# Optimization experiments

Hardware: AMD Instinct MI355X
Metric: run time of the kernel (lower is better)

Reference implementation:

```python
import jax, jax.numpy as jnp
import numpy as np

F_OUT = 256      # out_channels
NH = 8           # num_heads
DH = F_OUT // NH # head dim = 32
KH = KW = 8      # kernel (window) size == stride == q_stride
KK = KH * KW     # 64 keys per window


def setup_inputs() -> dict:
    key = jax.random.key(0)
    k1, k2, k3 = jax.random.split(key, 3)
    x = jax.random.normal(k1, (8, 256, 128, 128), jnp.float32)
    # 1x1 conv weight for qkv projection, xavier-ish scale
    proj_w = jax.random.normal(k2, (3 * F_OUT, 256), jnp.float32) * (1.0 / np.sqrt(256.0))
    proj_b = jnp.zeros((3 * F_OUT,), jnp.float32)
    # learned position features (module inits to zeros; use small random for a nontrivial test)
    pos_feats = jax.random.normal(k3, (F_OUT, KK), jnp.float32) * 0.02
    return {"x": x, "proj_w": proj_w, "proj_b": proj_b, "pos_feats": pos_feats}


def reference(x, proj_w, proj_b, pos_feats):
    B, C, H, W = x.shape
    f = F_OUT
    # 1x1 conv == channel GEMM: [B,3f,H,W]
    qkv = jnp.einsum('bchw,oc->bohw', x, proj_w) + proj_b[None, :, None, None]
    scale = float(f // NH) ** (-0.25)
    # query: slice every q_stride-th position -> [B,f,Hq,Wq]
    q = qkv[:, :f, ::KH, ::KW]
    kv = qkv[:, f:3 * f]                       # [B,2f,H,W]
    Hq, Wq = H // KH, W // KW
    # non-overlapping window unfold (stride==kernel, padding=0, dilation=1)
    # -> [B,Hq,Wq,2f,KK], matching torch as_strided(...).reshape(..., -1)
    kv = kv.reshape(B, 2 * f, Hq, KH, Wq, KW)
    kv = kv.transpose(0, 2, 4, 1, 3, 5).reshape(B, Hq, Wq, 2 * f, KK)
    # keys: pos_feats + scale*key, then split heads -> [B,Hq,Wq,NH,DH,KK]
    key_m = (pos_feats + scale * kv[..., :f, :]).reshape(B, Hq, Wq, NH, DH, KK)
    val_m = kv[..., f:2 * f, :].reshape(B, Hq, Wq, NH, DH, KK)
    # queries: scale, channels-last, split heads -> [B,Hq,Wq,NH,DH]
    q_m = (scale * q).transpose(0, 2, 3, 1).reshape(B, Hq, Wq, NH, DH)
    logits = jnp.einsum('bhwnd,bhwndk->bhwnk', q_m, key_m)   # [B,Hq,Wq,NH,KK]
    attn = jax.nn.softmax(logits, axis=-1)
    out = jnp.einsum('bhwnk,bhwndk->bhwnd', attn, val_m)     # [B,Hq,Wq,NH,DH]
    return out.reshape(B, Hq, Wq, f).transpose(0, 3, 1, 2)   # [B,f,Hq,Wq]
```

## Files before the change

kernel.cpp:

```cpp
#include <hip/hip_runtime.h>
#include <hip/hip_bf16.h>
#include <cstdint>
#include <cstddef>

#define SCALE 0.42044820762685725f

typedef __attribute__((ext_vector_type(8))) short short8;
typedef __attribute__((ext_vector_type(4))) short short4v;
typedef __attribute__((ext_vector_type(4))) float f32x4;

__device__ __forceinline__ unsigned int pk2bf(float lo, float hi) {
    __hip_bfloat162 h = __float22bfloat162_rn(float2{lo, hi});
    unsigned int u;
    __builtin_memcpy(&u, &h, sizeof(u));
    return u;
}
__device__ __forceinline__ unsigned short f2bf(float f) {
    unsigned int u = __builtin_bit_cast(unsigned int, f);
    u = (u + 0x7fffu + ((u >> 16) & 1u)) >> 16;
    return (unsigned short)u;
}
__device__ __forceinline__ float bf2f(unsigned short h) {
    unsigned int u = ((unsigned int)h) << 16;
    return __builtin_bit_cast(float, u);
}


__global__ __launch_bounds__(256) void prepack_w(const float* __restrict__ w,
                                                 const float* __restrict__ pos,
                                                 unsigned short* __restrict__ wp,
                                                 unsigned short* __restrict__ pT,
                                                 float* __restrict__ wqT) {
    int gid = blockIdx.x * 256 + threadIdx.x;
    if (gid < 24576) {
        int lane = gid & 63;
        int ks   = (gid >> 6) & 7;
        int mtg  = gid >> 9;
        int row  = (mtg < 32 ? 256 + mtg * 16 : (mtg - 32) * 16) + (lane & 15);
        int k0   = ks * 32 + (lane >> 4) * 8;
        const float* src = w + row * 256 + k0;
        short8 v;
#pragma unroll
        for (int j = 0; j < 8; ++j) v[j] = (short)f2bf(src[j]);
        *reinterpret_cast<short8*>(wp + (size_t)gid * 8) = v;
    } else if (gid < 40960) {
        int u = gid - 24576;
        pT[u] = f2bf(pos[(u & 255) * 64 + (u >> 8)]);
    } else {
        int u = gid - 40960;
        wqT[u] = w[(u & 255) * 256 + (u >> 8)];
    }
}

__global__ __launch_bounds__(256) void q_kernel(const float* __restrict__ x,
                                                const float* __restrict__ wqT,
                                                const float* __restrict__ proj_b,
                                                float* __restrict__ q_all) {
    __shared__ float s_x0[16][256];
    const int t = threadIdx.x;
    const int tile0 = blockIdx.x * 16;
    const int b = tile0 >> 8, hq = (tile0 >> 4) & 15;
    {
        const float* src = x + (size_t)b * 4194304 + (size_t)t * 16384 + hq * 1024;
#pragma unroll
        for (int j = 0; j < 16; ++j) s_x0[j][t] = src[j * 8];
    }
    __syncthreads();
    float acc[16];
#pragma unroll
    for (int j = 0; j < 16; ++j) acc[j] = 0.f;
#pragma unroll 4
    for (int c = 0; c < 256; ++c) {
        float wv = wqT[c * 256 + t];
#pragma unroll
        for (int j = 0; j < 16; ++j) acc[j] = fmaf(wv, s_x0[j][c], acc[j]);
    }
    float bq = proj_b[t];
#pragma unroll
    for (int j = 0; j < 16; ++j)
        q_all[(size_t)(tile0 + j) * 256 + t] = SCALE * (acc[j] + bq);
}

template <bool PRE>
__global__ __launch_bounds__(512, 2) void attn_fused(
        const float* __restrict__ x, const float* __restrict__ proj_w,
        const float* __restrict__ proj_b, const float* __restrict__ pos,
        const unsigned short* __restrict__ wpack, const unsigned short* __restrict__ posT,
        const float* __restrict__ q_all, float* __restrict__ out) {
    __shared__ __align__(16) unsigned char s_x[4][32768];
    __shared__ __align__(16) float s_vbias[256];
    __shared__ __align__(16) float s_qs[256];

    const int t    = threadIdx.x;
    const int lane = t & 63;
    const int wave = t >> 6;
    const int l15  = lane & 15;
    const int l4   = lane >> 4;

    const int bid   = blockIdx.x;
    const int b     = bid & 7;
    const int strip = bid >> 3;
    const int hq    = strip >> 2;
    const int wq0   = (strip & 3) * 4;
    const int tile0 = b * 256 + hq * 16 + wq0;

    if (t < 256) s_vbias[t] = proj_b[512 + t];

    short4v pos4[4][2];
    if (PRE) {
#pragma unroll
        for (int nt = 0; nt < 4; ++nt)
#pragma unroll
            for (int mt = 0; mt < 2; ++mt)
                pos4[nt][mt] = *reinterpret_cast<const short4v*>(
                    posT + (size_t)(nt * 16 + l15) * 256 + wave * 32 + mt * 16 + l4 * 4);
    }

    {
        const int pl  = lane & 1;
        const int w2  = (lane >> 1) & 15;
        const int hlo = (lane >> 5) & 1;
        const int pxs = w2 * 2 + pl;
        const int til = pxs >> 3;
        const int px7 = pxs & 7;
        const float* xs = x + (size_t)b * 4194304 + (size_t)(hq * 8) * 128 + wq0 * 8;
#pragma unroll 1
        for (int kb = 0; kb < 8; ++kb) {
            float2 v[8];
#pragma unroll
            for (int u = 0; u < 8; ++u) {
                int idx = wave * 64 + kb * 8 + u;
                int c   = (idx & 127) * 2 + pl;
                int h   = (idx >> 7) * 2 + hlo;
                v[u] = *reinterpret_cast<const float2*>(xs + (size_t)c * 16384 + h * 128 + w2 * 2);
            }
#pragma unroll
            for (int u = 0; u < 8; ++u) {
                int idx = wave * 64 + kb * 8 + u;
                int h   = (idx >> 7) * 2 + hlo;
                int pin = h * 8 + px7;
                float sel   = pl ? v[u].x : v[u].y;
                float other = __shfl_xor(sel, 1);
                unsigned int pk = pl ? pk2bf(other, v[u].y) : pk2bf(v[u].x, other);
                *reinterpret_cast<unsigned int*>(
                    s_x[til] + pin * 512 + ((4 * (idx & 127)) ^ ((pin & 7) << 4))) = pk;
            }
        }
    }
    __syncthreads();

#pragma unroll 1
    for (int ti = 0; ti < 4; ++ti) {
        const int tile = tile0 + ti;
        const int wq   = wq0 + ti;
        const unsigned char* xl = s_x[ti];

        f32x4 acc[4][4];
#pragma unroll
        for (int mt = 0; mt < 4; ++mt)
#pragma unroll
            for (int nt = 0; nt < 4; ++nt) acc[mt][nt] = (f32x4){0.f, 0.f, 0.f, 0.f};
        f32x4 accQ[2];
        if (!PRE) {
#pragma unroll
            for (int mt = 0; mt < 2; ++mt) accQ[mt] = (f32x4){0.f, 0.f, 0.f, 0.f};
        }

#pragma unroll 2
        for (int ks = 0; ks < 8; ++ks) {
            short8 bfr[4];
#pragma unroll
            for (int nt = 0; nt < 4; ++nt) {
                int n  = nt * 16 + l15;
                int kb = ks * 32 + l4 * 8;
                bfr[nt] = *reinterpret_cast<const short8*>(
                    xl + n * 512 + ((2 * kb) ^ ((n & 7) << 4)));
            }
            short8 afk[2], afv[2];
#pragma unroll
            for (int mt = 0; mt < 2; ++mt) {
                if (PRE) {
                    afk[mt] = *reinterpret_cast<const short8*>(
                        wpack + ((size_t)(((wave * 2 + mt) * 8 + ks) * 64 + lane)) * 8);
                    afv[mt] = *reinterpret_cast<const short8*>(
                        wpack + ((size_t)(((16 + wave * 2 + mt) * 8 + ks) * 64 + lane)) * 8);
                } else {
                    const float* wk = proj_w + (256 + (wave * 2 + mt) * 16 + l15) * 256 + ks * 32 + l4 * 8;
                    const float* wv = proj_w + (512 + (wave * 2 + mt) * 16 + l15) * 256 + ks * 32 + l4 * 8;
#pragma unroll
                    for (int j = 0; j < 8; ++j) { afk[mt][j] = (short)f2bf(wk[j]); afv[mt][j] = (short)f2bf(wv[j]); }
                }
            }
#pragma unroll
            for (int mt = 0; mt < 2; ++mt)
#pragma unroll
                for (int nt = 0; nt < 4; ++nt) {
                    acc[mt][nt]     = __builtin_amdgcn_mfma_f32_16x16x32_bf16(afk[mt], bfr[nt], acc[mt][nt], 0, 0, 0);
                    acc[2 + mt][nt] = __builtin_amdgcn_mfma_f32_16x16x32_bf16(afv[mt], bfr[nt], acc[2 + mt][nt], 0, 0, 0);
                }
            if (!PRE) {
                short8 afq[2];
#pragma unroll
                for (int mt = 0; mt < 2; ++mt) {
                    const float* wq2 = proj_w + ((wave * 2 + mt) * 16 + l15) * 256 + ks * 32 + l4 * 8;
#pragma unroll
                    for (int j = 0; j < 8; ++j) afq[mt][j] = (short)f2bf(wq2[j]);
                    accQ[mt] = __builtin_amdgcn_mfma_f32_16x16x32_bf16(afq[mt], bfr[0], accQ[mt], 0, 0, 0);
                }
            }
        }

        if (!PRE) {
            if (l15 == 0) {
#pragma unroll
                for (int mt = 0; mt < 2; ++mt)
#pragma unroll
                    for (int i = 0; i < 4; ++i) {
                        int row = wave * 32 + mt * 16 + l4 * 4 + i;
                        s_qs[row] = SCALE * (accQ[mt][i] + proj_b[row]);
                    }
            }
        }

        float attnw[4];
        {
            float qf[2][4];
            if (PRE) {
                const float* qp = q_all + (size_t)tile * 256 + wave * 32 + l4 * 4;
#pragma unroll
                for (int mt = 0; mt < 2; ++mt) {
                    float4 qv = *reinterpret_cast<const float4*>(qp + mt * 16);
                    qf[mt][0] = qv.x; qf[mt][1] = qv.y; qf[mt][2] = qv.z; qf[mt][3] = qv.w;
                }
            } else {
#pragma unroll
                for (int mt = 0; mt < 2; ++mt)
#pragma unroll
                    for (int i = 0; i < 4; ++i) qf[mt][i] = s_qs[wave * 32 + mt * 16 + l4 * 4 + i];
            }

            float lg[4];
#pragma unroll
            for (int nt = 0; nt < 4; ++nt) {
                float p = 0.f;
#pragma unroll
                for (int mt = 0; mt < 2; ++mt)
#pragma unroll
                    for (int i = 0; i < 4; ++i) {
                        float pf = PRE ? bf2f((unsigned short)pos4[nt][mt][i])
                                       : pos[(size_t)(wave * 32 + mt * 16 + l4 * 4 + i) * 64 + nt * 16 + l15];
                        p = fmaf(qf[mt][i], fmaf(SCALE, acc[mt][nt][i], pf), p);
                    }
                p += __shfl_xor(p, 16);
                p += __shfl_xor(p, 32);
                lg[nt] = p;
            }
            float mx = fmaxf(fmaxf(lg[0], lg[1]), fmaxf(lg[2], lg[3]));
            mx = fmaxf(mx, __shfl_xor(mx, 1));
            mx = fmaxf(mx, __shfl_xor(mx, 2));
            mx = fmaxf(mx, __shfl_xor(mx, 4));
            mx = fmaxf(mx, __shfl_xor(mx, 8));
            float e0 = __expf(lg[0] - mx), e1 = __expf(lg[1] - mx);
            float e2 = __expf(lg[2] - mx), e3 = __expf(lg[3] - mx);
            float s = (e0 + e1) + (e2 + e3);
            s += __shfl_xor(s, 1);
            s += __shfl_xor(s, 2);
            s += __shfl_xor(s, 4);
            s += __shfl_xor(s, 8);
            float rs = 1.f / s;
            attnw[0] = e0 * rs; attnw[1] = e1 * rs; attnw[2] = e2 * rs; attnw[3] = e3 * rs;
        }

#pragma unroll
        for (int mt = 0; mt < 2; ++mt) {
#pragma unroll
            for (int i = 0; i < 4; ++i) {
                float sum = attnw[0] * acc[2 + mt][0][i] + attnw[1] * acc[2 + mt][1][i]
                          + attnw[2] * acc[2 + mt][2][i] + attnw[3] * acc[2 + mt][3][i];
                sum += __shfl_xor(sum, 1);
                sum += __shfl_xor(sum, 2);
                sum += __shfl_xor(sum, 4);
                sum += __shfl_xor(sum, 8);
                if (l15 == 0) {
                    int vr = wave * 32 + mt * 16 + l4 * 4 + i;
                    out[(size_t)b * 65536 + (size_t)vr * 256 + hq * 16 + wq] = sum + s_vbias[vr];
                }
            }
        }
    }
}

extern "C" void kernel_launch(void* const* d_in, const int* in_sizes, int n_in,
                              void* d_out, int out_size, void* d_ws, size_t ws_size,
                              hipStream_t stream) {
    (void)in_sizes; (void)n_in; (void)out_size;
    const float* x      = (const float*)d_in[0];
    const float* proj_w = (const float*)d_in[1];
    const float* proj_b = (const float*)d_in[2];
    const float* pos    = (const float*)d_in[3];
    float* out = (float*)d_out;

    const size_t OFF_POST = 393216;
    const size_t OFF_WQT  = 425984;
    const size_t OFF_QALL = 688128;
    const size_t need_ws  = OFF_QALL + 2097152;

    if (d_ws != nullptr && ws_size >= need_ws) {
        unsigned short* wp  = (unsigned short*)d_ws;
        unsigned short* pT  = (unsigned short*)((char*)d_ws + OFF_POST);
        float*          wqT = (float*)((char*)d_ws + OFF_WQT);
        float*          qA  = (float*)((char*)d_ws + OFF_QALL);
        prepack_w<<<416, 256, 0, stream>>>(proj_w, pos, wp, pT, wqT);
        q_kernel<<<128, 256, 0, stream>>>(x, wqT, proj_b, qA);
        attn_fused<true><<<512, 512, 0, stream>>>(x, proj_w, proj_b, pos, wp, pT, qA, out);
    } else {
        attn_fused<false><<<512, 512, 0, stream>>>(x, proj_w, proj_b, pos, nullptr, nullptr, nullptr, out);
    }
}
```

Measured before the change: 102.5 us.

## Halve tiles per block to double grid and raise occupancy

Each block now handles 2 window tiles instead of 4. That halves the LDS staging buffer to 64KB and doubles the grid to 1024 blocks, with launch bounds raised to 4 blocks per CU. The x staging load is rewritten to issue all 32 float2 loads up front and pair channels with a shuffle across 8 lanes. The pos fragment load is moved inside the tile loop to cut register pressure. This aims at more resident waves and better latency hiding, at the cost of reloading pos per tile and a heavier register demand from the 32-entry load buffer.

```diff
diff --git a/kernel.cpp b/kernel.cpp
--- a/kernel.cpp
+++ b/kernel.cpp
@@ -82,12 +82,12 @@
 }
 
 template <bool PRE>
-__global__ __launch_bounds__(512, 2) void attn_fused(
+__global__ __launch_bounds__(512, 4) void attn_fused(
         const float* __restrict__ x, const float* __restrict__ proj_w,
         const float* __restrict__ proj_b, const float* __restrict__ pos,
         const unsigned short* __restrict__ wpack, const unsigned short* __restrict__ posT,
         const float* __restrict__ q_all, float* __restrict__ out) {
-    __shared__ __align__(16) unsigned char s_x[4][32768];
+    __shared__ __align__(16) unsigned char s_x[2][32768];
     __shared__ __align__(16) float s_vbias[256];
     __shared__ __align__(16) float s_qs[256];
 
@@ -100,57 +100,45 @@
     const int bid   = blockIdx.x;
     const int b     = bid & 7;
     const int strip = bid >> 3;
-    const int hq    = strip >> 2;
-    const int wq0   = (strip & 3) * 4;
+    const int hq    = strip >> 3;
+    const int wq0   = (strip & 7) * 2;
     const int tile0 = b * 256 + hq * 16 + wq0;
 
     if (t < 256) s_vbias[t] = proj_b[512 + t];
 
-    short4v pos4[4][2];
-    if (PRE) {
-#pragma unroll
-        for (int nt = 0; nt < 4; ++nt)
-#pragma unroll
-            for (int mt = 0; mt < 2; ++mt)
-                pos4[nt][mt] = *reinterpret_cast<const short4v*>(
-                    posT + (size_t)(nt * 16 + l15) * 256 + wave * 32 + mt * 16 + l4 * 4);
-    }
-
     {
-        const int pl  = lane & 1;
-        const int w2  = (lane >> 1) & 15;
-        const int hlo = (lane >> 5) & 1;
-        const int pxs = w2 * 2 + pl;
-        const int til = pxs >> 3;
-        const int px7 = pxs & 7;
-        const float* xs = x + (size_t)b * 4194304 + (size_t)(hq * 8) * 128 + wq0 * 8;
+        const int c3 = (lane >> 3) & 7;
+        const int w3 = lane & 7;
+        const int p  = c3 & 1;
+        const float* xs = x + (size_t)b * 4194304 + (size_t)(hq * 8) * 128 + wq0 * 8 + w3 * 2;
+        float2 v[32];
+#pragma unroll
+        for (int i = 0; i < 4; ++i)
+#pragma unroll
+            for (int h = 0; h < 8; ++h) {
+                int c = (i * 8 + wave) * 8 + c3;
+                v[i * 8 + h] = *reinterpret_cast<const float2*>(xs + (size_t)c * 16384 + h * 128);
+            }
+#pragma unroll
+        for (int i = 0; i < 4; ++i)
+#pragma unroll
+            for (int h = 0; h < 8; ++h) {
+                float2 w2 = v[i * 8 + h];
+                float sel   = p ? w2.x : w2.y;
+                float other = __shfl_xor(sel, 8);
+                unsigned int pk = p ? pk2bf(other, w2.y) : pk2bf(w2.x, other);
+                int px    = w3 * 2 + p;
+                int til   = px >> 3;
+                int pin   = h * 8 + (px & 7);
+                int cpair = (i * 8 + wave) * 4 + (c3 >> 1);
+                *reinterpret_cast<unsigned int*>(
+                    s_x[til] + pin * 512 + ((4 * cpair) ^ ((pin & 7) << 4))) = pk;
+            }
+    }
+    __syncthreads();
+
 #pragma unroll 1
-        for (int kb = 0; kb < 8; ++kb) {
-            float2 v[8];
-#pragma unroll
-            for (int u = 0; u < 8; ++u) {
-                int idx = wave * 64 + kb * 8 + u;
-                int c   = (idx & 127) * 2 + pl;
-                int h   = (idx >> 7) * 2 + hlo;
-                v[u] = *reinterpret_cast<const float2*>(xs + (size_t)c * 16384 + h * 128 + w2 * 2);
-            }
-#pragma unroll
-            for (int u = 0; u < 8; ++u) {
-                int idx = wave * 64 + kb * 8 + u;
-                int h   = (idx >> 7) * 2 + hlo;
-                int pin = h * 8 + px7;
-                float sel   = pl ? v[u].x : v[u].y;
-                float other = __shfl_xor(sel, 1);
-                unsigned int pk = pl ? pk2bf(other, v[u].y) : pk2bf(v[u].x, other);
-                *reinterpret_cast<unsigned int*>(
-                    s_x[til] + pin * 512 + ((4 * (idx & 127)) ^ ((pin & 7) << 4))) = pk;
-            }
-        }
-    }
-    __syncthreads();
-
-#pragma unroll 1
-    for (int ti = 0; ti < 4; ++ti) {
+    for (int ti = 0; ti < 2; ++ti) {
         const int tile = tile0 + ti;
         const int wq   = wq0 + ti;
         const unsigned char* xl = s_x[ti];
@@ -237,6 +225,15 @@
                 for (int mt = 0; mt < 2; ++mt)
 #pragma unroll
                     for (int i = 0; i < 4; ++i) qf[mt][i] = s_qs[wave * 32 + mt * 16 + l4 * 4 + i];
+            }
+            short4v pos4[4][2];
+            if (PRE) {
+#pragma unroll
+                for (int nt = 0; nt < 4; ++nt)
+#pragma unroll
+                    for (int mt = 0; mt < 2; ++mt)
+                        pos4[nt][mt] = *reinterpret_cast<const short4v*>(
+                            posT + (size_t)(nt * 16 + l15) * 256 + wave * 32 + mt * 16 + l4 * 4);
             }
 
             float lg[4];
@@ -312,8 +309,8 @@
         float*          qA  = (float*)((char*)d_ws + OFF_QALL);
         prepack_w<<<416, 256, 0, stream>>>(proj_w, pos, wp, pT, wqT);
         q_kernel<<<128, 256, 0, stream>>>(x, wqT, proj_b, qA);
-        attn_fused<true><<<512, 512, 0, stream>>>(x, proj_w, proj_b, pos, wp, pT, qA, out);
+        attn_fused<true><<<1024, 512, 0, stream>>>(x, proj_w, proj_b, pos, wp, pT, qA, out);
     } else {
-        attn_fused<false><<<512, 512, 0, stream>>>(x, proj_w, proj_b, pos, nullptr, nullptr, nullptr, out);
-    }
-}
+        attn_fused<false><<<1024, 512, 0, stream>>>(x, proj_w, proj_b, pos, nullptr, nullptr, nullptr, out);
+    }
+}
```

Measured after the change: 137.2 us. +33.8%, slower.
